# Performance work log

Measured on AMD Instinct MI355X. Metric: run time of the kernel, lower is better.

Reference implementation:

```python
import jax, jax.numpy as jnp
import numpy as np

# static config (matches init_kwargs)
E = 1280          # n_embed
L = 4             # n_layer
NH = 16           # n_heads
D = E // NH       # head_dim = 80
M = 5120          # n_mlp
O = 2048          # n_output_embed
MS = 2            # spatial_merge_size
NGPS = 48         # sqrt(num_position_embeddings)
GRID_T, GRID_H, GRID_W = 1, 32, 32
N_IMG = 2
SPP = GRID_T * GRID_H * GRID_W   # 1024 tokens per image
S = N_IMG * SPP                  # 2048 total tokens
H4 = E * MS * MS                 # merger hidden = 5120
IN_PATCH = 3 * 2 * 16 * 16       # 1536
DS_IDX = [1, 2]


def _ln(x, w, b, eps=1e-6):
    m = x.mean(-1, keepdims=True)
    v = ((x - m) ** 2).mean(-1, keepdims=True)
    return (x - m) / jnp.sqrt(v + eps) * w + b


def _pos_embed_interp(pos_emb):
    # bilinear interpolation of the 48x48 learned grid to GRID_HxGRID_W, per image
    hi = jnp.linspace(0.0, NGPS - 1.0, GRID_H)
    wi = jnp.linspace(0.0, NGPS - 1.0, GRID_W)
    hf = hi.astype(jnp.int32); wf = wi.astype(jnp.int32)
    hc = jnp.minimum(hf + 1, NGPS - 1); wc = jnp.minimum(wf + 1, NGPS - 1)
    dh = hi - hf; dw = wi - wf
    idx = [(hf[:, None] * NGPS + wf[None]).ravel(), (hf[:, None] * NGPS + wc[None]).ravel(),
           (hc[:, None] * NGPS + wf[None]).ravel(), (hc[:, None] * NGPS + wc[None]).ravel()]
    wts = [((1 - dh)[:, None] * (1 - dw)[None]).ravel(), ((1 - dh)[:, None] * dw[None]).ravel(),
           (dh[:, None] * (1 - dw)[None]).ravel(), (dh[:, None] * dw[None]).ravel()]
    pe = sum(pos_emb[i] * w[:, None] for i, w in zip(idx, wts))  # [h*w, E]
    pe = jnp.tile(pe, (GRID_T, 1))
    # spatial-merge permutation: (t, h/m, m, w/m, m) -> (t, h/m, w/m, m, m)
    pe = pe.reshape(GRID_T, GRID_H // MS, MS, GRID_W // MS, MS, E).transpose(0, 1, 3, 2, 4, 5).reshape(-1, E)
    return jnp.tile(pe, (N_IMG, 1))  # [S, E]


def _rotary_freqs():
    dim = D // 2  # VisionRotaryEmbedding dim = 40
    inv = 1.0 / (10000.0 ** (jnp.arange(0, dim, 2, dtype=jnp.float32) / dim))  # [D//4]
    hp = jnp.broadcast_to(jnp.arange(GRID_H)[:, None], (GRID_H, GRID_W))
    hp = hp.reshape(GRID_H // MS, MS, GRID_W // MS, MS).transpose(0, 2, 1, 3).ravel()
    wp = jnp.broadcast_to(jnp.arange(GRID_W)[None, :], (GRID_H, GRID_W))
    wp = wp.reshape(GRID_H // MS, MS, GRID_W // MS, MS).transpose(0, 2, 1, 3).ravel()
    pos = jnp.stack([hp, wp], -1)            # [h*w, 2]
    pos = jnp.tile(pos, (GRID_T, 1))
    pos = jnp.tile(pos, (N_IMG, 1))          # [S, 2]
    table = jnp.arange(max(GRID_H, GRID_W), dtype=jnp.float32)[:, None] * inv[None]  # [G, D//4]
    return table[pos].reshape(S, -1)         # [S, D//2] (h-freqs || w-freqs)


def _rope(t, cos, sin):
    # t: [S, NH, D]; cos/sin: [S, 1, D]; applied in float32 as in the source
    t1, t2 = jnp.split(t, 2, axis=-1)
    rot = jnp.concatenate([-t2, t1], -1)
    return (t.astype(jnp.float32) * cos + rot.astype(jnp.float32) * sin).astype(t.dtype)


def _attn(x, qkv_w, qkv_b, pw, pb, cos, sin, mask):
    qkv = (x @ qkv_w.T + qkv_b).reshape(S, 3, NH, D)
    q, k, v = qkv[:, 0], qkv[:, 1], qkv[:, 2]
    q = _rope(q, cos, sin)
    k = _rope(k, cos, sin)
    scores = jnp.einsum('shd,thd->hst', q, k) / np.sqrt(D).astype(np.float32) + mask
    p = jax.nn.softmax(scores.astype(jnp.float32), axis=-1).astype(q.dtype)
    o = jnp.einsum('hst,thd->shd', p, v).reshape(S, E)
    return o @ pw.T + pb


def _merger(x, ln_w, ln_b, f1w, f1b, f2w, f2b, post):
    if post:
        x = _ln(x.reshape(-1, H4), ln_w, ln_b)
    else:
        x = _ln(x, ln_w, ln_b).reshape(-1, H4)
    h = jax.nn.gelu(x @ f1w.T + f1b, approximate=False)  # nn.GELU() exact
    return h @ f2w.T + f2b


def setup_inputs() -> dict:
    key = jax.random.key(0)
    ks = iter(jax.random.split(key, 24))
    n = lambda s: jax.random.normal(next(ks), s, dtype=jnp.float32) * 0.02
    return {
        'x': jax.random.normal(next(ks), (S, IN_PATCH), dtype=jnp.float32),
        'patch_w': n((E, IN_PATCH)), 'patch_b': jnp.zeros((E,), jnp.float32),
        'pos_emb': n((NGPS * NGPS, E)),
        'ln1_w': jnp.ones((L, E), jnp.float32), 'ln1_b': jnp.zeros((L, E), jnp.float32),
        'ln2_w': jnp.ones((L, E), jnp.float32), 'ln2_b': jnp.zeros((L, E), jnp.float32),
        'qkv_w': n((L, 3 * E, E)), 'qkv_b': jnp.zeros((L, 3 * E), jnp.float32),
        'attn_proj_w': n((L, E, E)), 'attn_proj_b': jnp.zeros((L, E), jnp.float32),
        'fc1_w': n((L, M, E)), 'fc1_b': jnp.zeros((L, M), jnp.float32),
        'fc2_w': n((L, E, M)), 'fc2_b': jnp.zeros((L, E), jnp.float32),
        'm_ln_w': jnp.ones((E,), jnp.float32), 'm_ln_b': jnp.zeros((E,), jnp.float32),
        'm_fc1_w': n((H4, H4)), 'm_fc1_b': jnp.zeros((H4,), jnp.float32),
        'm_fc2_w': n((O, H4)), 'm_fc2_b': jnp.zeros((O,), jnp.float32),
        'ds_ln_w': jnp.ones((2, H4), jnp.float32), 'ds_ln_b': jnp.zeros((2, H4), jnp.float32),
        'ds_fc1_w': n((2, H4, H4)), 'ds_fc1_b': jnp.zeros((2, H4), jnp.float32),
        'ds_fc2_w': n((2, O, H4)), 'ds_fc2_b': jnp.zeros((2, O), jnp.float32),
    }


def reference(x, patch_w, patch_b, pos_emb, ln1_w, ln1_b, ln2_w, ln2_b,
              qkv_w, qkv_b, attn_proj_w, attn_proj_b, fc1_w, fc1_b, fc2_w, fc2_b,
              m_ln_w, m_ln_b, m_fc1_w, m_fc1_b, m_fc2_w, m_fc2_b,
              ds_ln_w, ds_ln_b, ds_fc1_w, ds_fc1_b, ds_fc2_w, ds_fc2_b):
    # patch embed (Conv3d with kernel==stride == per-patch linear)
    h = x @ patch_w.T + patch_b                      # [S, E]
    h = h + _pos_embed_interp(pos_emb)
    freqs = _rotary_freqs()                          # [S, D//2]
    cos = jnp.concatenate([jnp.cos(freqs)] * 2, -1)[:, None, :]  # [S,1,D]
    sin = jnp.concatenate([jnp.sin(freqs)] * 2, -1)[:, None, :]
    img = jnp.arange(S) // SPP                       # cu_seqlens block-diagonal mask
    mask = jnp.where(img[:, None] == img[None, :], 0.0, jnp.finfo(jnp.float32).min)
    ds_feats = []
    for l in range(L):
        h = h + _attn(_ln(h, ln1_w[l], ln1_b[l]), qkv_w[l], qkv_b[l],
                      attn_proj_w[l], attn_proj_b[l], cos, sin, mask)
        hn = _ln(h, ln2_w[l], ln2_b[l])
        h = h + (jax.nn.gelu(hn @ fc1_w[l].T + fc1_b[l], approximate=True) @ fc2_w[l].T + fc2_b[l])
        if l in DS_IDX:
            j = DS_IDX.index(l)
            ds_feats.append(_merger(h, ds_ln_w[j], ds_ln_b[j], ds_fc1_w[j], ds_fc1_b[j],
                                    ds_fc2_w[j], ds_fc2_b[j], post=True))
    main = _merger(h, m_ln_w, m_ln_b, m_fc1_w, m_fc1_b, m_fc2_w, m_fc2_b, post=False)
    return jnp.stack([main] + ds_feats, 0)           # [3, S//4, O]
```

## Files before the change

### kernel.cpp

```cpp
#include <hip/hip_runtime.h>
#include <hip/hip_bf16.h>
#include <cstdio>
#include <cstdint>

#define E_    1280
#define L_    4
#define NH_   16
#define D_    80
#define DP_   96
#define MLP_  5120
#define O_    2048
#define S_    2048
#define H4_   5120
#define INP_  1536

typedef __attribute__((ext_vector_type(4))) float f32x4;
typedef __attribute__((ext_vector_type(8))) short short8v;
typedef __attribute__((ext_vector_type(4))) short short4v;

__device__ __forceinline__ short f2bf(float f){
  uint32_t u = __float_as_uint(f);
  uint32_t r = (u + 0x7FFFu + ((u >> 16) & 1u)) >> 16;
  return (short)r;
}
__device__ __forceinline__ float bf2f(short s){
  return __uint_as_float(((uint32_t)(uint16_t)s) << 16);
}
__device__ __forceinline__ float gelu_tanh(float x){
  return 0.5f*x*(1.f + tanhf(0.7978845608028654f*(x + 0.044715f*x*x*x)));
}
__device__ __forceinline__ float gelu_erf(float x){
  return 0.5f*x*(1.f + erff(x*0.7071067811865476f));
}
__device__ __forceinline__ void token_hw(int t, int& hc, int& wc){
  hc = ((t>>1)&1) + ((t>>6)<<1);
  wc = (t&1)      + (((t>>2)&15)<<1);
}

__device__ __forceinline__ void gload16(const short* g, short* l){
  __builtin_amdgcn_global_load_lds((const __attribute__((address_space(1))) void*)g,
                                   (__attribute__((address_space(3))) void*)l, 16, 0, 0);
}

__global__ __launch_bounds__(256)
void cvt_k(const float* __restrict__ src, short* __restrict__ dst, long long n)
{
  const long long stride = (long long)gridDim.x*256*8;
  for (long long i = ((long long)blockIdx.x*256 + threadIdx.x)*8; i < n; i += stride){
    float4 v0 = *(const float4*)(src+i);
    float4 v1 = *(const float4*)(src+i+4);
    short8v w;
    w[0]=f2bf(v0.x); w[1]=f2bf(v0.y); w[2]=f2bf(v0.z); w[3]=f2bf(v0.w);
    w[4]=f2bf(v1.x); w[5]=f2bf(v1.y); w[6]=f2bf(v1.z); w[7]=f2bf(v1.w);
    *(short8v*)(dst+i) = w;
  }
}

struct Gemm2P {
  const short* A; const short* B; void* C;
  const float* bias;
  short* part;
  int lda, ldb, ldc, M, N, K;
  float scale;
  long long aOffH, aOffI, bOffH, bOffI, cOffH, cOffI;
  int nImg, kSplit;
};

template<int EPI, bool RES, bool CF32, bool SPLIT>
__global__ __launch_bounds__(256)
void gemm2_k(Gemm2P p)
{
  __shared__ short As[3][4096];
  __shared__ short Bs[3][4096];

  int z = blockIdx.z, ks = 0;
  if constexpr (SPLIT){ ks = z % p.kSplit; z /= p.kSplit; }
  const int hI = z / p.nImg, iI = z % p.nImg;
  const long long aB = (long long)hI*p.aOffH + (long long)iI*p.aOffI;
  const long long bB = (long long)hI*p.bOffH + (long long)iI*p.bOffI;
  const long long cB = (long long)hI*p.cOffH + (long long)iI*p.cOffI;

  const int nwg = gridDim.x*gridDim.y;
  const int orig = blockIdx.y*gridDim.x + blockIdx.x;
  const int q8 = nwg >> 3, r8 = nwg & 7;
  const int xcd = orig & 7, oidx = orig >> 3;
  const int wg = (xcd < r8 ? xcd*(q8+1) : r8*(q8+1) + (xcd-r8)*q8) + oidx;
  const int nt = wg % gridDim.x, mt = wg / gridDim.x;

  const int tid = threadIdx.x, lane = tid & 63, wv = tid >> 6;

  const int sr = lane >> 2;
  const int sc = (lane & 3) * 8;
  const int Kp  = SPLIT ? p.K / p.kSplit : p.K;
  const int kBeg = SPLIT ? ks * Kp : 0;
  int ra0 = mt*128 + (wv*2+0)*16 + sr; if (ra0 >= p.M) ra0 = p.M-1;
  int ra1 = mt*128 + (wv*2+1)*16 + sr; if (ra1 >= p.M) ra1 = p.M-1;
  int rb0 = nt*128 + (wv*2+0)*16 + sr; if (rb0 >= p.N) rb0 = p.N-1;
  int rb1 = nt*128 + (wv*2+1)*16 + sr; if (rb1 >= p.N) rb1 = p.N-1;
  const short* pa0 = p.A + aB + (long long)ra0*p.lda + sc + kBeg;
  const short* pa1 = p.A + aB + (long long)ra1*p.lda + sc + kBeg;
  const short* pb0 = p.B + bB + (long long)rb0*p.ldb + sc + kBeg;
  const short* pb1 = p.B + bB + (long long)rb1*p.ldb + sc + kBeg;
  const int so0 = (wv*2+0)*512;
  const int so1 = (wv*2+1)*512;

  const int fr = lane & 15, fo = (lane >> 4) * 8;
  const int wr = (wv >> 1) * 64, wc = (wv & 1) * 64;

  f32x4 acc[4][4] = {};

  auto stage = [&](int buf, int t){
    const int k0 = t << 5;
    gload16(pa0 + k0, &As[buf][so0]);
    gload16(pa1 + k0, &As[buf][so1]);
    gload16(pb0 + k0, &Bs[buf][so0]);
    gload16(pb1 + k0, &Bs[buf][so1]);
  };

  const int ntile = Kp >> 5;
  stage(0, 0);
  if (ntile > 1) stage(1, 1);
  for (int t = 0; t < ntile; t++){
    const int cur = t % 3;
    if (t + 1 < ntile) { asm volatile("s_waitcnt vmcnt(4)" ::: "memory"); }
    else               { asm volatile("s_waitcnt vmcnt(0)" ::: "memory"); }
    __builtin_amdgcn_s_barrier();
    asm volatile("" ::: "memory");
    short8v a[4], b[4];
    #pragma unroll
    for (int i=0;i<4;i++){
      a[i] = *(const short8v*)&As[cur][(wr + i*16 + fr)*32 + fo];
      b[i] = *(const short8v*)&Bs[cur][(wc + i*16 + fr)*32 + fo];
    }
    if (t + 2 < ntile) stage((t+2)%3, t+2);
    #pragma unroll
    for (int i=0;i<4;i++)
      #pragma unroll
      for (int j=0;j<4;j++)
        acc[i][j] = __builtin_amdgcn_mfma_f32_16x16x32_bf16(a[i], b[j], acc[i][j], 0, 0, 0);
  }

  #pragma unroll
  for (int i=0;i<4;i++){
    #pragma unroll
    for (int j=0;j<4;j++){
      #pragma unroll
      for (int r=0;r<4;r++){
        const int row = mt*128 + wr + i*16 + (lane>>4)*4 + r;
        const int col = nt*128 + wc + j*16 + fr;
        if (row < p.M && col < p.N){
          float v = acc[i][j][r];
          if constexpr (SPLIT){
            p.part[((long long)ks*p.M + row)*p.N + col] = f2bf(v);
          } else {
            if (p.bias) v += p.bias[col];
            if constexpr (EPI==1) v = gelu_tanh(v);
            if constexpr (EPI==2) v = gelu_erf(v);
            if constexpr (EPI==3) v *= p.scale;
            const long long off = cB + (long long)row*p.ldc + col;
            if constexpr (RES)  v += ((const float*)p.C)[off];
            if constexpr (CF32) ((float*)p.C)[off] = v;
            else                ((short*)p.C)[off] = f2bf(v);
          }
        }
      }
    }
  }
}

template<int EPI, bool RES, bool CF32>
__global__ __launch_bounds__(256)
void reduce_k(const short* __restrict__ part, int kSplit, long long MN, int N,
              const float* __restrict__ bias, void* __restrict__ C)
{
  const long long i = ((long long)blockIdx.x*256 + threadIdx.x)*8;
  if (i >= MN) return;
  float v[8];
  { short8v pv = *(const short8v*)(part + i);
    #pragma unroll
    for (int e=0;e<8;e++) v[e] = bf2f(pv[e]); }
  for (int ks = 1; ks < kSplit; ks++){
    short8v pv = *(const short8v*)(part + (long long)ks*MN + i);
    #pragma unroll
    for (int e=0;e<8;e++) v[e] += bf2f(pv[e]);
  }
  if (bias){
    const int col = (int)(i % N);
    #pragma unroll
    for (int e=0;e<8;e++) v[e] += bias[col+e];
  }
  #pragma unroll
  for (int e=0;e<8;e++){
    if constexpr (EPI==1) v[e] = gelu_tanh(v[e]);
    if constexpr (EPI==2) v[e] = gelu_erf(v[e]);
  }
  if constexpr (RES){
    const float* cp = (const float*)C + i;
    #pragma unroll
    for (int e=0;e<8;e++) v[e] += cp[e];
  }
  if constexpr (CF32){
    float4 o0 = {v[0],v[1],v[2],v[3]}, o1 = {v[4],v[5],v[6],v[7]};
    *(float4*)((float*)C + i) = o0;
    *(float4*)((float*)C + i + 4) = o1;
  } else {
    short8v o;
    #pragma unroll
    for (int e=0;e<8;e++) o[e] = f2bf(v[e]);
    *(short8v*)((short*)C + i) = o;
  }
}

__global__ __launch_bounds__(256)
void redln_k(const short* __restrict__ part, long long MN, const float* __restrict__ bias,
             float* __restrict__ h, const float* __restrict__ lnw, const float* __restrict__ lnb,
             short* __restrict__ aln)
{
  __shared__ float red[8];
  const int row = blockIdx.x, tid = threadIdx.x;
  float4 vals[2];
  float s = 0.f, sq = 0.f;
  #pragma unroll
  for (int it=0; it<2; it++){
    const int c = tid*4 + it*1024;
    if (c < E_){
      float4 v = *(const float4*)(h + (long long)row*E_ + c);
      const float4 b = *(const float4*)(bias + c);
      v.x += b.x; v.y += b.y; v.z += b.z; v.w += b.w;
      #pragma unroll
      for (int ks=0; ks<4; ks++){
        short4v pv = *(const short4v*)(part + (long long)ks*MN + (long long)row*E_ + c);
        v.x += bf2f(pv[0]); v.y += bf2f(pv[1]); v.z += bf2f(pv[2]); v.w += bf2f(pv[3]);
      }
      *(float4*)(h + (long long)row*E_ + c) = v;
      vals[it] = v;
      s  += v.x+v.y+v.z+v.w;
      sq += v.x*v.x+v.y*v.y+v.z*v.z+v.w*v.w;
    }
  }
  #pragma unroll
  for (int m=32;m;m>>=1){ s += __shfl_xor(s,m,64); sq += __shfl_xor(sq,m,64); }
  const int wv = tid>>6, lane = tid&63;
  if (lane==0){ red[wv]=s; red[4+wv]=sq; }
  __syncthreads();
  s  = red[0]+red[1]+red[2]+red[3];
  sq = red[4]+red[5]+red[6]+red[7];
  const float mean = s / (float)E_;
  const float var  = sq / (float)E_ - mean*mean;
  const float rs   = rsqrtf(var + 1e-6f);
  #pragma unroll
  for (int it=0; it<2; it++){
    const int c = tid*4 + it*1024;
    if (c < E_){
      const float4 v = vals[it];
      const float4 gw = *(const float4*)(lnw + c);
      const float4 bw = *(const float4*)(lnb + c);
      short4v o;
      o[0] = f2bf((v.x-mean)*rs*gw.x + bw.x);
      o[1] = f2bf((v.y-mean)*rs*gw.y + bw.y);
      o[2] = f2bf((v.z-mean)*rs*gw.z + bw.z);
      o[3] = f2bf((v.w-mean)*rs*gw.w + bw.w);
      *(short4v*)(aln + (long long)row*E_ + c) = o;
    }
  }
}

__global__ __launch_bounds__(256)
void fattn_k(const short* __restrict__ qh, const short* __restrict__ kh,
             const short* __restrict__ vt, short* __restrict__ o2)
{
  __shared__ short Ps[4][16*136];

  const int qt = blockIdx.x, h = blockIdx.y, img = blockIdx.z;
  const int tid = threadIdx.x, lane = tid & 63, wv = tid >> 6;
  const int fr = lane & 15, fo = (lane >> 4) * 8, g = lane >> 4;

  const short* qp = qh + ((long long)h*S_ + img*1024 + qt*64 + wv*16)*DP_;
  const short* kp = kh + ((long long)h*S_ + img*1024)*DP_;
  const short* vp = vt + ((long long)(h*2 + img))*80*1024;
  short* Pw = &Ps[wv][0];

  short8v q[3];
  #pragma unroll
  for (int t3=0;t3<3;t3++)
    q[t3] = *(const short8v*)(qp + (long long)fr*DP_ + t3*32 + fo);

  float m_[4], l_[4];
  f32x4 ao[5] = {};
  #pragma unroll
  for (int r=0;r<4;r++){ m_[r] = -3.0e38f; l_[r] = 0.f; }

  for (int t = 0; t < 8; t++){
    f32x4 sc[8] = {};
    #pragma unroll
    for (int j=0;j<8;j++){
      #pragma unroll
      for (int t3=0;t3<3;t3++){
        const short8v kb = *(const short8v*)(kp + (long long)(t*128 + j*16 + fr)*DP_ + t3*32 + fo);
        sc[j] = __builtin_amdgcn_mfma_f32_16x16x32_bf16(q[t3], kb, sc[j], 0,0,0);
      }
    }
    #pragma unroll
    for (int j=0;j<8;j++) sc[j] *= 0.11180339887498949f;

    #pragma unroll
    for (int r=0;r<4;r++){
      float mx = sc[0][r];
      #pragma unroll
      for (int j=1;j<8;j++) mx = fmaxf(mx, sc[j][r]);
      mx = fmaxf(mx, __shfl_xor(mx, 1, 64));
      mx = fmaxf(mx, __shfl_xor(mx, 2, 64));
      mx = fmaxf(mx, __shfl_xor(mx, 4, 64));
      mx = fmaxf(mx, __shfl_xor(mx, 8, 64));
      const float mn = fmaxf(m_[r], mx);
      const float al = __expf(m_[r] - mn);
      float ts = 0.f;
      #pragma unroll
      for (int j=0;j<8;j++){
        const float pv = __expf(sc[j][r] - mn);
        sc[j][r] = pv;
        ts += pv;
      }
      ts += __shfl_xor(ts, 1, 64);
      ts += __shfl_xor(ts, 2, 64);
      ts += __shfl_xor(ts, 4, 64);
      ts += __shfl_xor(ts, 8, 64);
      l_[r] = l_[r]*al + ts;
      m_[r] = mn;
      #pragma unroll
      for (int n=0;n<5;n++) ao[n][r] *= al;
      const int prow = g*4 + r;
      #pragma unroll
      for (int j=0;j<8;j++) Pw[prow*136 + j*16 + fr] = f2bf(sc[j][r]);
    }
    asm volatile("s_waitcnt lgkmcnt(0)" ::: "memory");
    __builtin_amdgcn_sched_barrier(0);

    #pragma unroll
    for (int t4=0;t4<4;t4++){
      const short8v pa = *(const short8v*)&Pw[fr*136 + t4*32 + fo];
      #pragma unroll
      for (int n=0;n<5;n++){
        const short8v vb = *(const short8v*)(vp + (long long)(n*16 + fr)*1024 + t*128 + t4*32 + fo);
        ao[n] = __builtin_amdgcn_mfma_f32_16x16x32_bf16(pa, vb, ao[n], 0,0,0);
      }
    }
  }

  short* op = o2 + ((long long)(img*1024 + qt*64 + wv*16))*E_ + h*80;
  #pragma unroll
  for (int r=0;r<4;r++){
    const float inv = 1.f / l_[r];
    const int row = g*4 + r;
    #pragma unroll
    for (int n=0;n<5;n++)
      op[(long long)row*E_ + n*16 + fr] = f2bf(ao[n][r] * inv);
  }
}

__global__ __launch_bounds__(256)
void ln_k(const float* __restrict__ X, const float* __restrict__ g, const float* __restrict__ bta,
          short* __restrict__ Y, int Cn)
{
  __shared__ float red[8];
  const int row = blockIdx.x;
  const float* x = X + (long long)row*Cn;
  short* y = Y + (long long)row*Cn;
  float s = 0.f, sq = 0.f;
  for (int c = threadIdx.x*4; c < Cn; c += 1024){
    float4 v = *(const float4*)(x + c);
    s  += v.x+v.y+v.z+v.w;
    sq += v.x*v.x+v.y*v.y+v.z*v.z+v.w*v.w;
  }
  #pragma unroll
  for (int m=32;m;m>>=1){ s += __shfl_xor(s,m,64); sq += __shfl_xor(sq,m,64); }
  const int wv = threadIdx.x>>6, lane = threadIdx.x&63;
  if (lane==0){ red[wv]=s; red[4+wv]=sq; }
  __syncthreads();
  s  = red[0]+red[1]+red[2]+red[3];
  sq = red[4]+red[5]+red[6]+red[7];
  const float mean = s / (float)Cn;
  const float var  = sq / (float)Cn - mean*mean;
  const float rs   = rsqrtf(var + 1e-6f);
  for (int c = threadIdx.x*4; c < Cn; c += 1024){
    float4 v  = *(const float4*)(x + c);
    float4 gw = *(const float4*)(g + c);
    float4 bw = *(const float4*)(bta + c);
    short4v o;
    o[0] = f2bf((v.x-mean)*rs*gw.x + bw.x);
    o[1] = f2bf((v.y-mean)*rs*gw.y + bw.y);
    o[2] = f2bf((v.z-mean)*rs*gw.z + bw.z);
    o[3] = f2bf((v.w-mean)*rs*gw.w + bw.w);
    *(short4v*)(y + c) = o;
  }
}

__global__ __launch_bounds__(256)
void rope_k(const short* __restrict__ qkv, short* __restrict__ qh,
            short* __restrict__ kh, short* __restrict__ vt)
{
  const int idx = blockIdx.x*256 + threadIdx.x;
  if (idx >= S_*NH_*40) return;
  const int d0 = idx % 40;
  const int h  = (idx / 40) % NH_;
  const int s  = idx / (40*NH_);
  const int t  = s & 1023, img = s >> 10;
  int hc, wc; token_hw(t, hc, wc);
  const int j  = d0 % 20;
  const float invf = exp2f(-0.66438561897747f * (float)j);
  const float pos  = (float)((d0 < 20) ? hc : wc);
  float sn, cs;
  __sincosf(pos * invf, &sn, &cs);
  const short* base = qkv + (long long)s*3840 + h*80;
  const float q1 = bf2f(base[d0]),      q2 = bf2f(base[d0+40]);
  const float k1 = bf2f(base[1280+d0]), k2 = bf2f(base[1280+d0+40]);
  const long long qo = ((long long)h*S_ + s)*DP_;
  qh[qo + d0]    = f2bf(q1*cs - q2*sn);
  qh[qo + d0+40] = f2bf(q2*cs + q1*sn);
  kh[qo + d0]    = f2bf(k1*cs - k2*sn);
  kh[qo + d0+40] = f2bf(k2*cs + k1*sn);
  if (d0 < 16){ qh[qo + 80 + d0] = 0; kh[qo + 80 + d0] = 0; }
  const long long vo = (((long long)h*2 + img)*80)*1024 + t;
  vt[vo + (long long)d0*1024]      = base[2560+d0];
  vt[vo + (long long)(d0+40)*1024] = base[2560+d0+40];
}

__global__ __launch_bounds__(256)
void posadd_k(float* __restrict__ h, const float* __restrict__ pe)
{
  const int idx = blockIdx.x*256 + threadIdx.x;
  if (idx >= S_*(E_/4)) return;
  const int c4 = idx % (E_/4), s = idx / (E_/4);
  const int e = c4*4;
  const int t = s & 1023;
  int hc, wc; token_hw(t, hc, wc);
  const float hi = (float)hc * (47.f/31.f);
  const float wi = (float)wc * (47.f/31.f);
  int hf = (int)hi; float dh = hi - (float)hf; int h2 = min(hf+1, 47);
  int wf = (int)wi; float dw = wi - (float)wf; int w2 = min(wf+1, 47);
  const float w00=(1.f-dh)*(1.f-dw), w01=(1.f-dh)*dw, w10=dh*(1.f-dw), w11=dh*dw;
  const float4 a = *(const float4*)(pe + ((long long)(hf*48+wf))*E_ + e);
  const float4 b = *(const float4*)(pe + ((long long)(hf*48+w2))*E_ + e);
  const float4 c = *(const float4*)(pe + ((long long)(h2*48+wf))*E_ + e);
  const float4 d = *(const float4*)(pe + ((long long)(h2*48+w2))*E_ + e);
  float* out = h + (long long)s*E_ + e;
  float4 o = *(float4*)out;
  o.x += w00*a.x + w01*b.x + w10*c.x + w11*d.x;
  o.y += w00*a.y + w01*b.y + w10*c.y + w11*d.y;
  o.z += w00*a.z + w01*b.z + w10*c.z + w11*d.z;
  o.w += w00*a.w + w01*b.w + w10*c.w + w11*d.w;
  *(float4*)out = o;
}

static Gemm2P mk(const short* A, const short* B, void* C, const float* bias,
                 int lda, int ldb, int ldc, int M, int N, int K, float scale = 1.f)
{
  Gemm2P p{}; p.A=A; p.B=B; p.C=C; p.bias=bias; p.part=nullptr;
  p.lda=lda; p.ldb=ldb; p.ldc=ldc; p.M=M; p.N=N; p.K=K; p.scale=scale;
  p.aOffH=p.aOffI=p.bOffH=p.bOffI=p.cOffH=p.cOffI=0; p.nImg=1; p.kSplit=1;
  return p;
}

extern "C" void kernel_launch(void* const* d_in, const int* in_sizes, int n_in,
                              void* d_out, int out_size, void* d_ws, size_t ws_size,
                              hipStream_t stream)
{
  const float* x           = (const float*)d_in[0];
  const float* patch_w     = (const float*)d_in[1];
  const float* patch_b     = (const float*)d_in[2];
  const float* pos_emb     = (const float*)d_in[3];
  const float* ln1_w       = (const float*)d_in[4];
  const float* ln1_b       = (const float*)d_in[5];
  const float* ln2_w       = (const float*)d_in[6];
  const float* ln2_b       = (const float*)d_in[7];
  const float* qkv_w       = (const float*)d_in[8];
  const float* qkv_b       = (const float*)d_in[9];
  const float* attn_proj_w = (const float*)d_in[10];
  const float* attn_proj_b = (const float*)d_in[11];
  const float* fc1_w       = (const float*)d_in[12];
  const float* fc1_b       = (const float*)d_in[13];
  const float* fc2_w       = (const float*)d_in[14];
  const float* fc2_b       = (const float*)d_in[15];
  const float* m_ln_w      = (const float*)d_in[16];
  const float* m_ln_b      = (const float*)d_in[17];
  const float* m_fc1_w     = (const float*)d_in[18];
  const float* m_fc1_b     = (const float*)d_in[19];
  const float* m_fc2_w     = (const float*)d_in[20];
  const float* m_fc2_b     = (const float*)d_in[21];
  const float* ds_ln_w     = (const float*)d_in[22];
  const float* ds_ln_b     = (const float*)d_in[23];
  const float* ds_fc1_w    = (const float*)d_in[24];
  const float* ds_fc1_b    = (const float*)d_in[25];
  const float* ds_fc2_w    = (const float*)d_in[26];
  const float* ds_fc2_b    = (const float*)d_in[27];
  float* out = (float*)d_out;

  char* wsp = (char*)d_ws;
  auto alloc = [&](size_t bytes)->char*{
    char* p = wsp; wsp += (bytes + 255) & ~(size_t)255; return p;
  };
  float* h    = (float*)alloc((size_t)S_*E_*4);
  short* qkvb = (short*)alloc((size_t)S_*3840*2);
  short* aln  = (short*)alloc((size_t)S_*E_*2);
  short* qh   = (short*)alloc((size_t)NH_*S_*DP_*2);
  short* kh   = (short*)alloc((size_t)NH_*S_*DP_*2 + 4096);
  short* vt   = (short*)alloc((size_t)NH_*2*D_*1024*2 + 4096);
  short* part = (short*)alloc((size_t)48*1024*1024);
  short* o2   = (short*)alloc((size_t)S_*E_*2);
  short* ffn  = (short*)alloc((size_t)S_*MLP_*2);
  short* xb    = (short*)alloc((size_t)S_*INP_*2);
  short* pwB   = (short*)alloc((size_t)E_*INP_*2);
  short* qkvwB = (short*)alloc((size_t)L_*3840*E_*2);
  short* prwB  = (short*)alloc((size_t)L_*E_*E_*2);
  short* f1wB  = (short*)alloc((size_t)L_*MLP_*E_*2);
  short* f2wB  = (short*)alloc((size_t)L_*E_*MLP_*2);
  short* mf1B  = (short*)alloc((size_t)H4_*H4_*2);
  short* mf2B  = (short*)alloc((size_t)O_*H4_*2);
  short* df1B  = (short*)alloc((size_t)2*H4_*H4_*2);
  short* df2B  = (short*)alloc((size_t)2*O_*H4_*2);
  size_t need = (size_t)(wsp - (char*)d_ws);
  if (need > ws_size){
    fprintf(stderr, "kernel_launch: ws too small: need %zu have %zu\n", need, ws_size);
    return;
  }
  short* dsln = qkvb;

  const dim3 B256(256);
  auto cvt = [&](const float* src, short* dst, long long n){
    unsigned blk = (unsigned)min((long long)8192, (n/8 + 255)/256);
    cvt_k<<<blk, B256, 0, stream>>>(src, dst, n);
  };
  cvt(x, xb, (long long)S_*INP_);
  cvt(patch_w, pwB, (long long)E_*INP_);
  cvt(qkv_w, qkvwB, (long long)L_*3840*E_);
  cvt(attn_proj_w, prwB, (long long)L_*E_*E_);
  cvt(fc1_w, f1wB, (long long)L_*MLP_*E_);
  cvt(fc2_w, f2wB, (long long)L_*E_*MLP_);
  cvt(m_fc1_w, mf1B, (long long)H4_*H4_);
  cvt(m_fc2_w, mf2B, (long long)O_*H4_);
  cvt(ds_fc1_w, df1B, (long long)2*H4_*H4_);
  cvt(ds_fc2_w, df2B, (long long)2*O_*H4_);

  auto G = [](int M, int N, int ks = 1){
    return dim3((unsigned)((N+127)/128), (unsigned)((M+127)/128), (unsigned)ks);
  };
  auto RG = [](long long MN){ return dim3((unsigned)((MN/8 + 255)/256)); };

  { Gemm2P pp = mk(xb, pwB, h, nullptr, INP_, INP_, E_, S_, E_, INP_);
    pp.part = part; pp.kSplit = 4;
    gemm2_k<0,false,true,true><<<G(S_,E_,4),B256,0,stream>>>(pp);
    reduce_k<0,false,true><<<RG((long long)S_*E_),B256,0,stream>>>(part, 4, (long long)S_*E_, E_, patch_b, h); }
  posadd_k<<<(S_*(E_/4)+255)/256, B256, 0, stream>>>(h, pos_emb);
  ln_k<<<S_, B256, 0, stream>>>(h, ln1_w, ln1_b, aln, E_);

  for (int l = 0; l < L_; l++){
    { Gemm2P pp = mk(aln, qkvwB + (size_t)l*3840*E_, qkvb, nullptr, E_, E_, 3840, S_, 3840, E_);
      pp.part = part; pp.kSplit = 2;
      gemm2_k<0,false,false,true><<<G(S_,3840,2),B256,0,stream>>>(pp);
      reduce_k<0,false,false><<<RG((long long)S_*3840),B256,0,stream>>>(part, 2, (long long)S_*3840, 3840, qkv_b + l*3840, qkvb); }
    rope_k<<<(S_*NH_*40+255)/256, B256, 0, stream>>>(qkvb, qh, kh, vt);
    fattn_k<<<dim3(16,16,2), B256, 0, stream>>>(qh, kh, vt, o2);
    { Gemm2P pp = mk(o2, prwB + (size_t)l*E_*E_, nullptr, nullptr, E_, E_, E_, S_, E_, E_);
      pp.part = part; pp.kSplit = 4;
      gemm2_k<0,false,true,true><<<G(S_,E_,4),B256,0,stream>>>(pp);
      redln_k<<<S_, B256, 0, stream>>>(part, (long long)S_*E_, attn_proj_b + l*E_,
                                       h, ln2_w + l*E_, ln2_b + l*E_, aln); }

    { Gemm2P pp = mk(aln, f1wB + (size_t)l*MLP_*E_, ffn, nullptr, E_, E_, MLP_, S_, MLP_, E_);
      pp.part = part; pp.kSplit = 2;
      gemm2_k<0,false,false,true><<<G(S_,MLP_,2),B256,0,stream>>>(pp);
      reduce_k<1,false,false><<<RG((long long)S_*MLP_),B256,0,stream>>>(part, 2, (long long)S_*MLP_, MLP_, fc1_b + l*MLP_, ffn); }
    { Gemm2P pp = mk(ffn, f2wB + (size_t)l*E_*MLP_, nullptr, nullptr, MLP_, MLP_, E_, S_, E_, MLP_);
      pp.part = part; pp.kSplit = 4;
      gemm2_k<0,false,true,true><<<G(S_,E_,4),B256,0,stream>>>(pp);
      const float* nw = (l < 3) ? (ln1_w + (l+1)*E_) : m_ln_w;
      const float* nb = (l < 3) ? (ln1_b + (l+1)*E_) : m_ln_b;
      redln_k<<<S_, B256, 0, stream>>>(part, (long long)S_*E_, fc2_b + l*E_, h, nw, nb, aln); }

    if (l == 1 || l == 2){
      const int j = l - 1;
      ln_k<<<512, B256, 0, stream>>>(h, ds_ln_w + (size_t)j*H4_, ds_ln_b + (size_t)j*H4_, dsln, H4_);
      { Gemm2P pp = mk(dsln, df1B + (size_t)j*H4_*H4_, ffn, nullptr, H4_, H4_, H4_, 512, H4_, H4_);
        pp.part = part; pp.kSplit = 4;
        gemm2_k<0,false,false,true><<<G(512,H4_,4),B256,0,stream>>>(pp);
        reduce_k<2,false,false><<<RG((long long)512*H4_),B256,0,stream>>>(part, 4, (long long)512*H4_, H4_, ds_fc1_b + (size_t)j*H4_, ffn); }
      { Gemm2P pp = mk(ffn, df2B + (size_t)j*O_*H4_, out + (size_t)(1+j)*512*O_, nullptr, H4_, H4_, O_, 512, O_, H4_);
        pp.part = part; pp.kSplit = 8;
        gemm2_k<0,false,true,true><<<G(512,O_,8),B256,0,stream>>>(pp);
        reduce_k<0,false,true><<<RG((long long)512*O_),B256,0,stream>>>(part, 8, (long long)512*O_, O_, ds_fc2_b + (size_t)j*O_, out + (size_t)(1+j)*512*O_); }
    }
  }

  { Gemm2P pp = mk(aln, mf1B, ffn, nullptr, H4_, H4_, H4_, 512, H4_, H4_);
    pp.part = part; pp.kSplit = 4;
    gemm2_k<0,false,false,true><<<G(512,H4_,4),B256,0,stream>>>(pp);
    reduce_k<2,false,false><<<RG((long long)512*H4_),B256,0,stream>>>(part, 4, (long long)512*H4_, H4_, m_fc1_b, ffn); }
  { Gemm2P pp = mk(ffn, mf2B, out, nullptr, H4_, H4_, O_, 512, O_, H4_);
    pp.part = part; pp.kSplit = 8;
    gemm2_k<0,false,true,true><<<G(512,O_,8),B256,0,stream>>>(pp);
    reduce_k<0,false,true><<<RG((long long)512*O_),B256,0,stream>>>(part, 8, (long long)512*O_, O_, m_fc2_b, out); }
}
```

Before: 1.773 ms.

## Fuse patch reduce, pos-embed and LN; drop split-K for QKV and FC1

Adds a redposln_k kernel that reduces the patch-embed split-K partials, adds the bias and the interpolated position embedding, and applies LayerNorm in one pass. This replaces three separate kernels and their round trips through h. The QKV and FC1 GEMMs now run without split-K, with bias and activation applied in the GEMM epilogue, so the partial-buffer write, read and reduce launches go away. GELU-tanh now uses an __expf-based formula. Trade-offs: the non-split GEMMs launch half as many blocks, and the exp form can overflow to inf/inf for large inputs.

```diff
diff --git a/kernel.cpp b/kernel.cpp
--- a/kernel.cpp
+++ b/kernel.cpp
@@ -27,7 +27,9 @@
   return __uint_as_float(((uint32_t)(uint16_t)s) << 16);
 }
 __device__ __forceinline__ float gelu_tanh(float x){
-  return 0.5f*x*(1.f + tanhf(0.7978845608028654f*(x + 0.044715f*x*x*x)));
+  const float z = 0.7978845608028654f*(x + 0.044715f*x*x*x);
+  const float e = __expf(2.f*z);
+  return 0.5f*x*(1.f + (e-1.f)/(e+1.f));
 }
 __device__ __forceinline__ float gelu_erf(float x){
   return 0.5f*x*(1.f + erff(x*0.7071067811865476f));
@@ -227,6 +229,80 @@
       float4 v = *(const float4*)(h + (long long)row*E_ + c);
       const float4 b = *(const float4*)(bias + c);
       v.x += b.x; v.y += b.y; v.z += b.z; v.w += b.w;
+      #pragma unroll
+      for (int ks=0; ks<4; ks++){
+        short4v pv = *(const short4v*)(part + (long long)ks*MN + (long long)row*E_ + c);
+        v.x += bf2f(pv[0]); v.y += bf2f(pv[1]); v.z += bf2f(pv[2]); v.w += bf2f(pv[3]);
+      }
+      *(float4*)(h + (long long)row*E_ + c) = v;
+      vals[it] = v;
+      s  += v.x+v.y+v.z+v.w;
+      sq += v.x*v.x+v.y*v.y+v.z*v.z+v.w*v.w;
+    }
+  }
+  #pragma unroll
+  for (int m=32;m;m>>=1){ s += __shfl_xor(s,m,64); sq += __shfl_xor(sq,m,64); }
+  const int wv = tid>>6, lane = tid&63;
+  if (lane==0){ red[wv]=s; red[4+wv]=sq; }
+  __syncthreads();
+  s  = red[0]+red[1]+red[2]+red[3];
+  sq = red[4]+red[5]+red[6]+red[7];
+  const float mean = s / (float)E_;
+  const float var  = sq / (float)E_ - mean*mean;
+  const float rs   = rsqrtf(var + 1e-6f);
+  #pragma unroll
+  for (int it=0; it<2; it++){
+    const int c = tid*4 + it*1024;
+    if (c < E_){
+      const float4 v = vals[it];
+      const float4 gw = *(const float4*)(lnw + c);
+      const float4 bw = *(const float4*)(lnb + c);
+      short4v o;
+      o[0] = f2bf((v.x-mean)*rs*gw.x + bw.x);
+      o[1] = f2bf((v.y-mean)*rs*gw.y + bw.y);
+      o[2] = f2bf((v.z-mean)*rs*gw.z + bw.z);
+      o[3] = f2bf((v.w-mean)*rs*gw.w + bw.w);
+      *(short4v*)(aln + (long long)row*E_ + c) = o;
+    }
+  }
+}
+
+__global__ __launch_bounds__(256)
+void redposln_k(const short* __restrict__ part, long long MN, const float* __restrict__ bias,
+                const float* __restrict__ pe, float* __restrict__ h,
+                const float* __restrict__ lnw, const float* __restrict__ lnb,
+                short* __restrict__ aln)
+{
+  __shared__ float red[8];
+  const int row = blockIdx.x, tid = threadIdx.x;
+  const int t = row & 1023;
+  int hc, wc; token_hw(t, hc, wc);
+  const float hi = (float)hc * (47.f/31.f);
+  const float wi = (float)wc * (47.f/31.f);
+  int hf = (int)hi; float dh = hi - (float)hf; int h2 = min(hf+1, 47);
+  int wf = (int)wi; float dw = wi - (float)wf; int w2 = min(wf+1, 47);
+  const float w00=(1.f-dh)*(1.f-dw), w01=(1.f-dh)*dw, w10=dh*(1.f-dw), w11=dh*dw;
+  const float* pe00 = pe + (long long)(hf*48+wf)*E_;
+  const float* pe01 = pe + (long long)(hf*48+w2)*E_;
+  const float* pe10 = pe + (long long)(h2*48+wf)*E_;
+  const float* pe11 = pe + (long long)(h2*48+w2)*E_;
+
+  float4 vals[2];
+  float s = 0.f, sq = 0.f;
+  #pragma unroll
+  for (int it=0; it<2; it++){
+    const int c = tid*4 + it*1024;
+    if (c < E_){
+      const float4 b = *(const float4*)(bias + c);
+      const float4 a0 = *(const float4*)(pe00 + c);
+      const float4 a1 = *(const float4*)(pe01 + c);
+      const float4 a2 = *(const float4*)(pe10 + c);
+      const float4 a3 = *(const float4*)(pe11 + c);
+      float4 v;
+      v.x = b.x + w00*a0.x + w01*a1.x + w10*a2.x + w11*a3.x;
+      v.y = b.y + w00*a0.y + w01*a1.y + w10*a2.y + w11*a3.y;
+      v.z = b.z + w00*a0.z + w01*a1.z + w10*a2.z + w11*a3.z;
+      v.w = b.w + w00*a0.w + w01*a1.w + w10*a2.w + w11*a3.w;
       #pragma unroll
       for (int ks=0; ks<4; ks++){
         short4v pv = *(const short4v*)(part + (long long)ks*MN + (long long)row*E_ + c);
@@ -423,33 +499,6 @@
   const long long vo = (((long long)h*2 + img)*80)*1024 + t;
   vt[vo + (long long)d0*1024]      = base[2560+d0];
   vt[vo + (long long)(d0+40)*1024] = base[2560+d0+40];
-}
-
-__global__ __launch_bounds__(256)
-void posadd_k(float* __restrict__ h, const float* __restrict__ pe)
-{
-  const int idx = blockIdx.x*256 + threadIdx.x;
-  if (idx >= S_*(E_/4)) return;
-  const int c4 = idx % (E_/4), s = idx / (E_/4);
-  const int e = c4*4;
-  const int t = s & 1023;
-  int hc, wc; token_hw(t, hc, wc);
-  const float hi = (float)hc * (47.f/31.f);
-  const float wi = (float)wc * (47.f/31.f);
-  int hf = (int)hi; float dh = hi - (float)hf; int h2 = min(hf+1, 47);
-  int wf = (int)wi; float dw = wi - (float)wf; int w2 = min(wf+1, 47);
-  const float w00=(1.f-dh)*(1.f-dw), w01=(1.f-dh)*dw, w10=dh*(1.f-dw), w11=dh*dw;
-  const float4 a = *(const float4*)(pe + ((long long)(hf*48+wf))*E_ + e);
-  const float4 b = *(const float4*)(pe + ((long long)(hf*48+w2))*E_ + e);
-  const float4 c = *(const float4*)(pe + ((long long)(h2*48+wf))*E_ + e);
-  const float4 d = *(const float4*)(pe + ((long long)(h2*48+w2))*E_ + e);
-  float* out = h + (long long)s*E_ + e;
-  float4 o = *(float4*)out;
-  o.x += w00*a.x + w01*b.x + w10*c.x + w11*d.x;
-  o.y += w00*a.y + w01*b.y + w10*c.y + w11*d.y;
-  o.z += w00*a.z + w01*b.z + w10*c.z + w11*d.z;
-  o.w += w00*a.w + w01*b.w + w10*c.w + w11*d.w;
-  *(float4*)out = o;
 }
 
 static Gemm2P mk(const short* A, const short* B, void* C, const float* bias,
@@ -546,18 +595,15 @@
   };
   auto RG = [](long long MN){ return dim3((unsigned)((MN/8 + 255)/256)); };
 
-  { Gemm2P pp = mk(xb, pwB, h, nullptr, INP_, INP_, E_, S_, E_, INP_);
+  { Gemm2P pp = mk(xb, pwB, nullptr, nullptr, INP_, INP_, E_, S_, E_, INP_);
     pp.part = part; pp.kSplit = 4;
     gemm2_k<0,false,true,true><<<G(S_,E_,4),B256,0,stream>>>(pp);
-    reduce_k<0,false,true><<<RG((long long)S_*E_),B256,0,stream>>>(part, 4, (long long)S_*E_, E_, patch_b, h); }
-  posadd_k<<<(S_*(E_/4)+255)/256, B256, 0, stream>>>(h, pos_emb);
-  ln_k<<<S_, B256, 0, stream>>>(h, ln1_w, ln1_b, aln, E_);
+    redposln_k<<<S_, B256, 0, stream>>>(part, (long long)S_*E_, patch_b, pos_emb,
+                                        h, ln1_w, ln1_b, aln); }
 
   for (int l = 0; l < L_; l++){
-    { Gemm2P pp = mk(aln, qkvwB + (size_t)l*3840*E_, qkvb, nullptr, E_, E_, 3840, S_, 3840, E_);
-      pp.part = part; pp.kSplit = 2;
-      gemm2_k<0,false,false,true><<<G(S_,3840,2),B256,0,stream>>>(pp);
-      reduce_k<0,false,false><<<RG((long long)S_*3840),B256,0,stream>>>(part, 2, (long long)S_*3840, 3840, qkv_b + l*3840, qkvb); }
+    { Gemm2P pp = mk(aln, qkvwB + (size_t)l*3840*E_, qkvb, qkv_b + l*3840, E_, E_, 3840, S_, 3840, E_);
+      gemm2_k<0,false,false,false><<<G(S_,3840),B256,0,stream>>>(pp); }
     rope_k<<<(S_*NH_*40+255)/256, B256, 0, stream>>>(qkvb, qh, kh, vt);
     fattn_k<<<dim3(16,16,2), B256, 0, stream>>>(qh, kh, vt, o2);
     { Gemm2P pp = mk(o2, prwB + (size_t)l*E_*E_, nullptr, nullptr, E_, E_, E_, S_, E_, E_);
@@ -566,10 +612,8 @@
       redln_k<<<S_, B256, 0, stream>>>(part, (long long)S_*E_, attn_proj_b + l*E_,
                                        h, ln2_w + l*E_, ln2_b + l*E_, aln); }
 
-    { Gemm2P pp = mk(aln, f1wB + (size_t)l*MLP_*E_, ffn, nullptr, E_, E_, MLP_, S_, MLP_, E_);
-      pp.part = part; pp.kSplit = 2;
-      gemm2_k<0,false,false,true><<<G(S_,MLP_,2),B256,0,stream>>>(pp);
-      reduce_k<1,false,false><<<RG((long long)S_*MLP_),B256,0,stream>>>(part, 2, (long long)S_*MLP_, MLP_, fc1_b + l*MLP_, ffn); }
+    { Gemm2P pp = mk(aln, f1wB + (size_t)l*MLP_*E_, ffn, fc1_b + l*MLP_, E_, E_, MLP_, S_, MLP_, E_);
+      gemm2_k<1,false,false,false><<<G(S_,MLP_),B256,0,stream>>>(pp); }
     { Gemm2P pp = mk(ffn, f2wB + (size_t)l*E_*MLP_, nullptr, nullptr, MLP_, MLP_, E_, S_, E_, MLP_);
       pp.part = part; pp.kSplit = 4;
       gemm2_k<0,false,true,true><<<G(S_,E_,4),B256,0,stream>>>(pp);
```

Result: faster. 1.688 ms (-4.7%).
